# Performance work log

Measured on AMD Instinct MI355X. Metric: run time of the kernel, lower is better.

## Reference

```python
import jax, jax.numpy as jnp
import numpy as np

NUM_E = 100000
NUM_R = 500
HIDDEN = 64
BATCH = 32
GAMMA = 12.0
EPSILON = 2.0
EMB_RANGE = (GAMMA + EPSILON) / HIDDEN  # 0.21875
PI = 3.141592653589793


def setup_inputs() -> dict:
    key = jax.random.key(0)
    k1, k2, k3 = jax.random.split(key, 3)
    facts = jax.random.randint(k1, (BATCH, 3), 0, 1000, dtype=jnp.int64)  # col0<num_e, col1<2*num_r
    entity_embedding = jax.random.uniform(
        k2, (NUM_E, 2 * HIDDEN), dtype=jnp.float32, minval=-EMB_RANGE, maxval=EMB_RANGE)
    relation_embedding = jax.random.uniform(
        k3, (NUM_R * 2, HIDDEN), dtype=jnp.float32, minval=-EMB_RANGE, maxval=EMB_RANGE)
    return {"facts": facts, "entity_embedding": entity_embedding,
            "relation_embedding": relation_embedding}


def reference(facts, entity_embedding, relation_embedding):
    # Gather head/relation embeddings for the batch
    head = entity_embedding[facts[:, 0]]          # [B, 2D]
    relation = relation_embedding[facts[:, 1]]    # [B, D]

    re_head, im_head = jnp.split(head, 2, axis=1)           # [B, D] each
    re_tail, im_tail = jnp.split(entity_embedding, 2, axis=1)  # [E, D] each

    phase = relation / (EMB_RANGE / PI)
    re_rel = jnp.cos(phase)
    im_rel = jnp.sin(phase)

    # Complex rotation of head by relation: [B, D]
    re_rot = re_head * re_rel - im_head * im_rel
    im_rot = re_head * im_rel + im_head * re_rel

    # Broadcast difference against all entities: [B, E, D]
    re_diff = re_rot[:, None, :] - re_tail[None, :, :]
    im_diff = im_rot[:, None, :] - im_tail[None, :, :]

    # Per-component complex modulus, summed over dim -> [B, E]
    dist = jnp.sqrt(re_diff * re_diff + im_diff * im_diff).sum(axis=2)
    return GAMMA - dist
```

## Files before the change

### kernel.cpp

```cpp
#include <hip/hip_runtime.h>
#include <math.h>

#define NUM_E   100000
#define GAMMA_F 12.0f
#define EMB_RANGE_F 0.21875f
#define INV_TWO_EMB (1.0f / (2.0f * EMB_RANGE_F))

typedef float v4f __attribute__((ext_vector_type(4)));
typedef float v2f __attribute__((ext_vector_type(2)));

static __device__ __forceinline__ v2f pk_sub(v2f a, v2f b) {
    v2f d;
    asm("v_pk_add_f32 %0, %1, %2 neg_lo:[0,1] neg_hi:[0,1]"
        : "=v"(d) : "v"(a), "v"(b));
    return d;
}
static __device__ __forceinline__ v2f pk_mul(v2f a, v2f b) {
    v2f d;
    asm("v_pk_mul_f32 %0, %1, %2" : "=v"(d) : "v"(a), "v"(b));
    return d;
}
static __device__ __forceinline__ v2f pk_fma(v2f a, v2f b, v2f c) {
    v2f d;
    asm("v_pk_fma_f32 %0, %1, %2, %3" : "=v"(d) : "v"(a), "v"(b), "v"(c));
    return d;
}
static __device__ __forceinline__ float sq2(v2f dx, v2f dy) {
    v2f sq = pk_fma(dy, dy, pk_mul(dx, dx));
    return __builtin_amdgcn_sqrtf(sq.x) + __builtin_amdgcn_sqrtf(sq.y);
}
static __device__ __forceinline__ v2f lo2(v4f v) { return __builtin_shufflevector(v, v, 0, 1); }
static __device__ __forceinline__ v2f hi2(v4f v) { return __builtin_shufflevector(v, v, 2, 3); }

template <int CTRL>
static __device__ __forceinline__ float dpp_xor_add(float x) {
    int y = __builtin_amdgcn_update_dpp(0, __float_as_int(x), CTRL, 0xF, 0xF, true);
    return x + __int_as_float(y);
}

static __device__ __forceinline__ float dist_entity(
        v4f er0, v4f er1, v4f ei0, v4f ei1,
        const v2f RR[4][4], const v2f RI[4][4], int dg) {
    v2f e2[4] = { lo2(er0), hi2(er0), lo2(er1), hi2(er1) };
    v2f i2[4] = { lo2(ei0), hi2(ei0), lo2(ei1), hi2(ei1) };
    float r[4];
#pragma unroll
    for (int kb = 0; kb < 4; ++kb) {
        float s0 = sq2(pk_sub(RR[kb][0], e2[0]), pk_sub(RI[kb][0], i2[0]));
        float s1 = sq2(pk_sub(RR[kb][1], e2[1]), pk_sub(RI[kb][1], i2[1]));
        float s2 = sq2(pk_sub(RR[kb][2], e2[2]), pk_sub(RI[kb][2], i2[2]));
        float s3 = sq2(pk_sub(RR[kb][3], e2[3]), pk_sub(RI[kb][3], i2[3]));
        float v = (s0 + s1) + (s2 + s3);
        v = dpp_xor_add<0xB1>(v);
        v = dpp_xor_add<0x4E>(v);
        v = dpp_xor_add<0x141>(v);
        r[kb] = v;
    }
    float sel = (dg == 0) ? r[0] : (dg == 1) ? r[1]
              : (dg == 2) ? r[2] : r[3];
    return GAMMA_F - sel;
}

#define LOADE(d0, d1, d2, d3, EIDX) do {                         \
    const float* _p = ent + (size_t)(EIDX) * 128 + dg * 8;       \
    d0 = *(const v4f*)(_p);      d1 = *(const v4f*)(_p + 4);     \
    d2 = *(const v4f*)(_p + 64); d3 = *(const v4f*)(_p + 68); } while (0)

__global__ __launch_bounds__(256, 2) void rotate_dist_fused(
        const int*   __restrict__ facts,
        const float* __restrict__ ent,
        const float* __restrict__ rel,
        float*       __restrict__ out) {
    __shared__ __align__(16) float rot_lds[16 * 64 * 4];

    const int t    = threadIdx.x;
    const int lane = t & 63;
    const int wv   = t >> 6;
    const int bg   = lane >> 3;
    const int dg   = lane & 7;

    {
        const int b  = bg * 4 + wv;
        const int f0 = facts[b * 3 + 0];
        const int f1 = facts[b * 3 + 1];
        const float* hp = ent + (size_t)f0 * 128 + dg * 8;
        const float* rp = rel + (size_t)f1 * 64  + dg * 8;
        v4f hre0 = *(const v4f*)(hp);
        v4f hre1 = *(const v4f*)(hp + 4);
        v4f him0 = *(const v4f*)(hp + 64);
        v4f him1 = *(const v4f*)(hp + 68);
        v4f ph0  = *(const v4f*)(rp);
        v4f ph1  = *(const v4f*)(rp + 4);
        v4f rr0, rr1, ri0, ri1;
#pragma unroll
        for (int j = 0; j < 4; ++j) {
            float rev0 = ph0[j] * INV_TWO_EMB;
            float s0 = __builtin_amdgcn_sinf(rev0);
            float c0 = __builtin_amdgcn_cosf(rev0);
            rr0[j] = hre0[j] * c0 - him0[j] * s0;
            ri0[j] = hre0[j] * s0 + him0[j] * c0;
            float rev1 = ph1[j] * INV_TWO_EMB;
            float s1 = __builtin_amdgcn_sinf(rev1);
            float c1 = __builtin_amdgcn_cosf(rev1);
            rr1[j] = hre1[j] * c1 - him1[j] * s1;
            ri1[j] = hre1[j] * s1 + him1[j] * c1;
        }
        float* wbase = rot_lds + (wv * 4) * 256 + lane * 4;
        *(v4f*)(wbase + 0 * 256) = rr0;
        *(v4f*)(wbase + 1 * 256) = rr1;
        *(v4f*)(wbase + 2 * 256) = ri0;
        *(v4f*)(wbase + 3 * 256) = ri1;
    }

    const int e0 = blockIdx.x * 32 + wv * 8;

    v4f A0, A1, A2, A3, B0, B1, B2, B3;
    LOADE(A0, A1, A2, A3, e0);

    __syncthreads();

    const float* rbase = rot_lds + lane * 4;
    float* obase = out + (size_t)(bg * 4 + (dg & 3)) * NUM_E + e0;

    v2f RR[4][4], RI[4][4];
#pragma unroll
    for (int kb = 0; kb < 4; ++kb) {
        v4f a = *(const v4f*)(rbase + (kb * 4 + 0) * 256);
        v4f b = *(const v4f*)(rbase + (kb * 4 + 1) * 256);
        v4f c = *(const v4f*)(rbase + (kb * 4 + 2) * 256);
        v4f d = *(const v4f*)(rbase + (kb * 4 + 3) * 256);
        RR[kb][0] = lo2(a); RR[kb][1] = hi2(a); RR[kb][2] = lo2(b); RR[kb][3] = hi2(b);
        RI[kb][0] = lo2(c); RI[kb][1] = hi2(c); RI[kb][2] = lo2(d); RI[kb][3] = hi2(d);
    }

    const int elast = NUM_E - 1;

#pragma unroll 1
    for (int g = 0; g < 2; ++g) {
        const int eb = e0 + g * 4;
        v4f vout;
        LOADE(B0, B1, B2, B3, eb + 1);
        vout[0] = dist_entity(A0, A1, A2, A3, RR, RI, dg);
        LOADE(A0, A1, A2, A3, eb + 2);
        vout[1] = dist_entity(B0, B1, B2, B3, RR, RI, dg);
        LOADE(B0, B1, B2, B3, eb + 3);
        vout[2] = dist_entity(A0, A1, A2, A3, RR, RI, dg);
        {
            int en = eb + 4; en = (en > elast) ? elast : en;
            LOADE(A0, A1, A2, A3, en);
        }
        vout[3] = dist_entity(B0, B1, B2, B3, RR, RI, dg);
        if (dg < 4) *(v4f*)(obase + g * 4) = vout;
    }
}

extern "C" void kernel_launch(void* const* d_in, const int* in_sizes, int n_in,
                              void* d_out, int out_size, void* d_ws, size_t ws_size,
                              hipStream_t stream) {
    const int*   facts = (const int*)d_in[0];
    const float* ent   = (const float*)d_in[1];
    const float* rel   = (const float*)d_in[2];
    float*       out   = (float*)d_out;
    (void)d_ws; (void)ws_size;

    rotate_dist_fused<<<dim3(NUM_E / 32), dim3(256), 0, stream>>>(facts, ent, rel, out);
}
```

Baseline: 119.4 us.

## Assign one batch row per lane group, dropping redundant per-batch compute and LDS

Each 8-lane group now owns a single batch row, so each thread computes one distance per entity instead of four and discarding three. The rotated head values stay in registers, which removes the shared-memory staging and the block barrier. Blocks cover 16 entities shared by all four waves, so entity rows are loaded redundantly by each wave and rely on cache hits. Output stores rotate across lanes by iteration.

```diff
diff --git a/kernel.cpp b/kernel.cpp
--- a/kernel.cpp
+++ b/kernel.cpp
@@ -40,25 +40,18 @@
 
 static __device__ __forceinline__ float dist_entity(
         v4f er0, v4f er1, v4f ei0, v4f ei1,
-        const v2f RR[4][4], const v2f RI[4][4], int dg) {
+        const v2f RR[4], const v2f RI[4]) {
     v2f e2[4] = { lo2(er0), hi2(er0), lo2(er1), hi2(er1) };
     v2f i2[4] = { lo2(ei0), hi2(ei0), lo2(ei1), hi2(ei1) };
-    float r[4];
-#pragma unroll
-    for (int kb = 0; kb < 4; ++kb) {
-        float s0 = sq2(pk_sub(RR[kb][0], e2[0]), pk_sub(RI[kb][0], i2[0]));
-        float s1 = sq2(pk_sub(RR[kb][1], e2[1]), pk_sub(RI[kb][1], i2[1]));
-        float s2 = sq2(pk_sub(RR[kb][2], e2[2]), pk_sub(RI[kb][2], i2[2]));
-        float s3 = sq2(pk_sub(RR[kb][3], e2[3]), pk_sub(RI[kb][3], i2[3]));
-        float v = (s0 + s1) + (s2 + s3);
-        v = dpp_xor_add<0xB1>(v);
-        v = dpp_xor_add<0x4E>(v);
-        v = dpp_xor_add<0x141>(v);
-        r[kb] = v;
-    }
-    float sel = (dg == 0) ? r[0] : (dg == 1) ? r[1]
-              : (dg == 2) ? r[2] : r[3];
-    return GAMMA_F - sel;
+    float s0 = sq2(pk_sub(RR[0], e2[0]), pk_sub(RI[0], i2[0]));
+    float s1 = sq2(pk_sub(RR[1], e2[1]), pk_sub(RI[1], i2[1]));
+    float s2 = sq2(pk_sub(RR[2], e2[2]), pk_sub(RI[2], i2[2]));
+    float s3 = sq2(pk_sub(RR[3], e2[3]), pk_sub(RI[3], i2[3]));
+    float v = (s0 + s1) + (s2 + s3);
+    v = dpp_xor_add<0xB1>(v);
+    v = dpp_xor_add<0x4E>(v);
+    v = dpp_xor_add<0x141>(v);
+    return GAMMA_F - v;
 }
 
 #define LOADE(d0, d1, d2, d3, EIDX) do {                         \
@@ -71,16 +64,19 @@
         const float* __restrict__ ent,
         const float* __restrict__ rel,
         float*       __restrict__ out) {
-    __shared__ __align__(16) float rot_lds[16 * 64 * 4];
-
     const int t    = threadIdx.x;
     const int lane = t & 63;
     const int wv   = t >> 6;
-    const int bg   = lane >> 3;
+    const int bq   = lane >> 3;
     const int dg   = lane & 7;
+    const int b    = wv * 8 + bq;
+    const int e0   = blockIdx.x * 16;
 
+    v4f A0, A1, A2, A3, B0, B1, B2, B3;
+    LOADE(A0, A1, A2, A3, e0);
+
+    v2f RR[4], RI[4];
     {
-        const int b  = bg * 4 + wv;
         const int f0 = facts[b * 3 + 0];
         const int f1 = facts[b * 3 + 1];
         const float* hp = ent + (size_t)f0 * 128 + dg * 8;
@@ -105,52 +101,29 @@
             rr1[j] = hre1[j] * c1 - him1[j] * s1;
             ri1[j] = hre1[j] * s1 + him1[j] * c1;
         }
-        float* wbase = rot_lds + (wv * 4) * 256 + lane * 4;
-        *(v4f*)(wbase + 0 * 256) = rr0;
-        *(v4f*)(wbase + 1 * 256) = rr1;
-        *(v4f*)(wbase + 2 * 256) = ri0;
-        *(v4f*)(wbase + 3 * 256) = ri1;
+        RR[0] = lo2(rr0); RR[1] = hi2(rr0); RR[2] = lo2(rr1); RR[3] = hi2(rr1);
+        RI[0] = lo2(ri0); RI[1] = hi2(ri0); RI[2] = lo2(ri1); RI[3] = hi2(ri1);
     }
 
-    const int e0 = blockIdx.x * 32 + wv * 8;
-
-    v4f A0, A1, A2, A3, B0, B1, B2, B3;
-    LOADE(A0, A1, A2, A3, e0);
-
-    __syncthreads();
-
-    const float* rbase = rot_lds + lane * 4;
-    float* obase = out + (size_t)(bg * 4 + (dg & 3)) * NUM_E + e0;
-
-    v2f RR[4][4], RI[4][4];
-#pragma unroll
-    for (int kb = 0; kb < 4; ++kb) {
-        v4f a = *(const v4f*)(rbase + (kb * 4 + 0) * 256);
-        v4f b = *(const v4f*)(rbase + (kb * 4 + 1) * 256);
-        v4f c = *(const v4f*)(rbase + (kb * 4 + 2) * 256);
-        v4f d = *(const v4f*)(rbase + (kb * 4 + 3) * 256);
-        RR[kb][0] = lo2(a); RR[kb][1] = hi2(a); RR[kb][2] = lo2(b); RR[kb][3] = hi2(b);
-        RI[kb][0] = lo2(c); RI[kb][1] = hi2(c); RI[kb][2] = lo2(d); RI[kb][3] = hi2(d);
-    }
-
+    float* obase = out + (size_t)b * NUM_E;
     const int elast = NUM_E - 1;
 
 #pragma unroll 1
-    for (int g = 0; g < 2; ++g) {
-        const int eb = e0 + g * 4;
+    for (int q = 0; q < 4; ++q) {
+        const int eb = e0 + q * 4;
         v4f vout;
         LOADE(B0, B1, B2, B3, eb + 1);
-        vout[0] = dist_entity(A0, A1, A2, A3, RR, RI, dg);
+        vout[0] = dist_entity(A0, A1, A2, A3, RR, RI);
         LOADE(A0, A1, A2, A3, eb + 2);
-        vout[1] = dist_entity(B0, B1, B2, B3, RR, RI, dg);
+        vout[1] = dist_entity(B0, B1, B2, B3, RR, RI);
         LOADE(B0, B1, B2, B3, eb + 3);
-        vout[2] = dist_entity(A0, A1, A2, A3, RR, RI, dg);
+        vout[2] = dist_entity(A0, A1, A2, A3, RR, RI);
         {
             int en = eb + 4; en = (en > elast) ? elast : en;
             LOADE(A0, A1, A2, A3, en);
         }
-        vout[3] = dist_entity(B0, B1, B2, B3, RR, RI, dg);
-        if (dg < 4) *(v4f*)(obase + g * 4) = vout;
+        vout[3] = dist_entity(B0, B1, B2, B3, RR, RI);
+        if (dg == q) *(v4f*)(obase + eb) = vout;
     }
 }
 
@@ -163,5 +136,5 @@
     float*       out   = (float*)d_out;
     (void)d_ws; (void)ws_size;
 
-    rotate_dist_fused<<<dim3(NUM_E / 32), dim3(256), 0, stream>>>(facts, ent, rel, out);
+    rotate_dist_fused<<<dim3(NUM_E / 16), dim3(256), 0, stream>>>(facts, ent, rel, out);
 }
```

Result: slower. 137.3 us (+15.0%).
